# Kernel optimization log

Measured on AMD Instinct MI355X. Metric: run time of the kernel, lower is better.

The kernel has to match this reference:

```python
import jax, jax.numpy as jnp
import numpy as np

B, C, H, W = 4, 256, 64, 64
IC = C // 2  # inter_channels default = in_channels // 2


def setup_inputs() -> dict:
    key = jax.random.key(0)
    ks = jax.random.split(key, 7)
    x = jax.random.normal(ks[0], (B, C, H, W), dtype=jnp.float32)
    s = 0.02
    Wq = jax.random.normal(ks[1], (IC, C), dtype=jnp.float32) * s
    bq = jnp.zeros((IC,), dtype=jnp.float32)
    Wk = jax.random.normal(ks[2], (IC, C), dtype=jnp.float32) * s
    bk = jnp.zeros((IC,), dtype=jnp.float32)
    Wv = jax.random.normal(ks[3], (C, C), dtype=jnp.float32) * s
    bv = jnp.zeros((C,), dtype=jnp.float32)
    gamma = jnp.full((1,), 0.1, dtype=jnp.float32)  # nn.Parameter; init 0 in torch, 0.1 here for nontrivial grads
    return {"x": x, "Wq": Wq, "bq": bq, "Wk": Wk, "bk": bk, "Wv": Wv, "bv": bv, "gamma": gamma}


def reference(x, Wq, bq, Wk, bk, Wv, bv, gamma):
    b, c, h, w = x.shape
    n = h * w
    # 1x1 conv projections == per-pixel linear layers
    q = jnp.einsum('bchw,oc->bohw', x, Wq) + bq[None, :, None, None]  # [B,IC,H,W]
    k = jnp.einsum('bchw,oc->bohw', x, Wk) + bk[None, :, None, None]
    v = jnp.einsum('bchw,oc->bohw', x, Wv) + bv[None, :, None, None]  # [B,C,H,W]
    q = q.reshape(b, IC, n).transpose(0, 2, 1)  # [B,N,IC]
    k = k.reshape(b, IC, n)                     # [B,IC,N]
    v = v.reshape(b, c, n)                      # [B,C,N]
    scale = jnp.asarray(IC, x.dtype) ** -0.5
    energy = jnp.einsum('bni,bim->bnm', q, k) * scale  # [B,N,N]
    attn = jax.nn.softmax(energy, axis=-1)             # dropout is identity in eval
    # torch: out = bmm(value, attention.transpose(-1,-2)) -> out[b,c,i] = sum_j v[b,c,j]*attn[b,i,j]
    out = jnp.einsum('bcj,bij->bci', v, attn).reshape(b, c, h, w)
    return gamma[0] * out + 2.0 * x
```

## Files before the change

### kernel.cpp

```cpp
#include <hip/hip_runtime.h>
#include <stdint.h>


#define Bn 4
#define Cn 256
#define ICn 128
#define Nn 4096

typedef __attribute__((ext_vector_type(8))) short bf16x8;
typedef __attribute__((ext_vector_type(4))) float f32x4;
typedef __attribute__((ext_vector_type(16))) float f32x16;
typedef __attribute__((ext_vector_type(8))) int i32x8;

#define SCALE1 0x7f7f7f7f

__device__ __forceinline__ unsigned short f2bf(float f) {
  union { float f; uint32_t u; } v; v.f = f;
  uint32_t r = (v.u + 0x7fffu + ((v.u >> 16) & 1u)) >> 16;
  return (unsigned short)r;
}

__device__ __forceinline__ uint32_t pk4_fp8(float a, float b, float c, float d) {
  int r = 0;
  r = __builtin_amdgcn_cvt_pk_fp8_f32(a, b, r, false);
  r = __builtin_amdgcn_cvt_pk_fp8_f32(c, d, r, true);
  return (uint32_t)r;
}

__global__ __launch_bounds__(256) void cvt_weights(const float* __restrict__ Wq,
                                                   const float* __restrict__ Wk,
                                                   const float* __restrict__ Wv,
                                                   unsigned short* __restrict__ wbf) {
  int t = blockIdx.x * 256 + threadIdx.x;
  int tile = t >> 9;
  int kk = (t >> 6) & 7;
  int lane = t & 63;
  const float* W; int row;
  if (tile < 8)       { W = Wq; row = tile * 16 + (lane & 15); }
  else if (tile < 16) { W = Wk; row = (tile - 8) * 16 + (lane & 15); }
  else                { W = Wv; row = (tile - 16) * 16 + (lane & 15); }
  const float* src = W + (size_t)row * Cn + kk * 32 + (lane >> 4) * 8;
  float4 f0 = *(const float4*)src;
  float4 f1 = *(const float4*)(src + 4);
  ushort4 o0, o1;
  o0.x = f2bf(f0.x); o0.y = f2bf(f0.y); o0.z = f2bf(f0.z); o0.w = f2bf(f0.w);
  o1.x = f2bf(f1.x); o1.y = f2bf(f1.y); o1.z = f2bf(f1.z); o1.w = f2bf(f1.w);
  *(ushort4*)(wbf + (size_t)t * 8)     = o0;
  *(ushort4*)(wbf + (size_t)t * 8 + 4) = o1;
}

__global__ __launch_bounds__(256, 2) void proj_kernel(const float* __restrict__ x,
                                                      const unsigned short* __restrict__ wbf,
                                                      const float* __restrict__ bq,
                                                      const float* __restrict__ bk,
                                                      const float* __restrict__ bv,
                                                      uint8_t* __restrict__ qF,
                                                      uint8_t* __restrict__ kF,
                                                      uint8_t* __restrict__ vF) {
  const int b = blockIdx.y;
  const int ntile = blockIdx.x;
  const int px0 = ntile * 32;
  const int tid = threadIdx.x;
  const int lane = tid & 63;
  const int w = tid >> 6;
  const int c0 = lane & 15, g = lane >> 4;
  const float hscale = 0.3570958292f;

  __shared__ __align__(16) unsigned short xT[32][264];
  __shared__ __align__(16) uint8_t tb[4][4096];

  #pragma unroll
  for (int t = 0; t < 8; ++t) {
    int c = (tid >> 3) + t * 32;
    int i8 = tid & 7;
    float4 f4 = *(const float4*)(x + ((size_t)(b * Cn + c)) * Nn + px0 + i8 * 4);
    xT[i8 * 4 + 0][c] = f2bf(f4.x);
    xT[i8 * 4 + 1][c] = f2bf(f4.y);
    xT[i8 * 4 + 2][c] = f2bf(f4.z);
    xT[i8 * 4 + 3][c] = f2bf(f4.w);
  }
  __syncthreads();

  bf16x8 a[2][8];
  #pragma unroll
  for (int h = 0; h < 2; ++h)
    #pragma unroll
    for (int kk = 0; kk < 8; ++kk)
      a[h][kk] = *(const bf16x8*)&xT[h * 16 + c0][kk * 32 + g * 8];

  f32x4 zero = {0.f, 0.f, 0.f, 0.f};
  uint8_t* tw = &tb[w][0];

  if (w < 2) {
    const int isq = (w == 0);
    const float* bias = isq ? bq : bk;
    uint8_t* dst = isq ? qF : kF;
    #pragma unroll
    for (int otl = 0; otl < 8; ++otl) {
      const int wt = (isq ? 0 : 8) + otl;
      bf16x8 wf[8];
      #pragma unroll
      for (int kk = 0; kk < 8; ++kk)
        wf[kk] = *(const bf16x8*)(wbf + (((size_t)wt * 8 + kk) << 9) + lane * 8);
      float4 bz = *(const float4*)(bias + otl * 16 + g * 4);
      #pragma unroll
      for (int h = 0; h < 2; ++h) {
        f32x4 acc = zero;
        #pragma unroll
        for (int kk = 0; kk < 8; ++kk)
          acc = __builtin_amdgcn_mfma_f32_16x16x32_bf16(wf[kk], a[h][kk], acc, 0, 0, 0);
        uint32_t d = pk4_fp8((acc[0] + bz.x) * hscale, (acc[1] + bz.y) * hscale,
                             (acc[2] + bz.z) * hscale, (acc[3] + bz.w) * hscale);
        int D = otl * 4 + g;
        int off = ((D >> 4) << 11) + (((((D >> 3) & 1) << 5) + h * 16 + c0) << 5) + ((D & 7) << 2);
        *(uint32_t*)(tw + off) = d;
      }
    }
    size_t base = ((size_t)(b * 128 + ntile)) << 12;
    #pragma unroll
    for (int r = 0; r < 4; ++r) {
      uint4 v = *(const uint4*)(tw + r * 1024 + lane * 16);
      *(uint4*)(dst + base + r * 1024 + lane * 16) = v;
    }
  } else {
    #pragma unroll
    for (int oi = 0; oi < 8; ++oi) {
      const int vtg = (w - 2) * 8 + oi;
      bf16x8 wf[8];
      #pragma unroll
      for (int kk = 0; kk < 8; ++kk)
        wf[kk] = *(const bf16x8*)(wbf + (((size_t)(16 + vtg) * 8 + kk) << 9) + lane * 8);
      const float bias = bv[vtg * 16 + c0];
      #pragma unroll
      for (int h = 0; h < 2; ++h) {
        f32x4 acc = zero;
        #pragma unroll
        for (int kk = 0; kk < 8; ++kk)
          acc = __builtin_amdgcn_mfma_f32_16x16x32_bf16(a[h][kk], wf[kk], acc, 0, 0, 0);
        uint32_t d = pk4_fp8(acc[0] + bias, acc[1] + bias, acc[2] + bias, acc[3] + bias);
        int off = (((vtg >> 1) & 3) << 10) + ((((vtg & 1) << 4) + c0) << 5) + ((h * 4 + g) << 2);
        *(uint32_t*)(tw + off) = d;
      }
    }
    const int ctb = (w - 2) * 4;
    size_t base0 = (((size_t)(b * 64 + (ntile >> 1)) * 8 + ctb) << 11)
                 + (size_t)(((ntile & 1) << 5) << 5);
    #pragma unroll
    for (int r = 0; r < 2; ++r) {
      int ctl = r * 2 + (lane >> 5);
      int li = lane & 31;
      const uint8_t* s = tw + r * 2048 + lane * 32;
      uint4 v0 = *(const uint4*)(s);
      uint4 v1 = *(const uint4*)(s + 16);
      uint8_t* gp = vF + base0 + ((size_t)ctl << 11) + li * 32;
      *(uint4*)(gp) = v0;
      *(uint4*)(gp + 16) = v1;
    }
  }
}

__global__ __launch_bounds__(256, 2) void attn_kernel(const uint8_t* __restrict__ qF,
                                                      const uint8_t* __restrict__ kF,
                                                      const uint8_t* __restrict__ vF,
                                                      const float* __restrict__ x,
                                                      const float* __restrict__ gamma,
                                                      float* __restrict__ out) {
  const int blk = blockIdx.x;
  const int b = (blk & 7) >> 1;
  const int rg = (blk >> 3) | ((blk & 1) << 6);
  const int n0 = rg * 32;
  const int ph = (blk >> 3) & 15;
  const int tid = threadIdx.x;
  const int L = tid & 63;
  const int ks = tid >> 6;
  const int l31 = L & 31, l5 = L >> 5;
  const bool lo = (l5 == 0);

  __shared__ __align__(16) struct SM {
    float obuf[256][33];
    float lsum[4][32];
  } sm;

  i32x8 qv[2];
  {
    const uint8_t* qp = qF + ((size_t)(b * 128 + rg) * 2) * 2048 + L * 32;
    #pragma unroll
    for (int mf = 0; mf < 2; ++mf) {
      union { uint4 u[2]; i32x8 v; } u;
      u.u[0] = *(const uint4*)(qp + mf * 2048);
      u.u[1] = *(const uint4*)(qp + mf * 2048 + 16);
      qv[mf] = u.v;
    }
  }

  f32x16 oacc[8];
  #pragma unroll
  for (int ct = 0; ct < 8; ++ct)
    #pragma unroll
    for (int i = 0; i < 16; ++i) oacc[ct][i] = 0.f;
  float lacc = 0.f;

  const uint8_t* kBase = kF + ((size_t)(b * 128) * 2) * 2048 + L * 32;
  const uint8_t* vBase = vF + ((size_t)(b * 64) * 8) * 2048 + L * 32;

  for (int it = 0; it < 16; ++it) {
    const int kb = ks * 16 + ((it + ph) & 15);

    i32x8 kv[4];
    {
      const uint8_t* kp = kBase + (size_t)kb * 8192;
      #pragma unroll
      for (int f = 0; f < 4; ++f) {
        union { uint4 u[2]; i32x8 v; } u;
        u.u[0] = *(const uint4*)(kp + f * 2048);
        u.u[1] = *(const uint4*)(kp + f * 2048 + 16);
        kv[f] = u.v;
      }
    }

    const uint8_t* vp = vBase + (size_t)kb * 16384;
    uint4 vA[8], vB[8];
    #pragma unroll
    for (int ct = 0; ct < 8; ++ct) vA[ct] = *(const uint4*)(vp + ct * 2048);

    f32x16 s;
    #pragma unroll
    for (int i = 0; i < 16; ++i) s[i] = 0.f;
    s = __builtin_amdgcn_mfma_scale_f32_32x32x64_f8f6f4(kv[0], qv[0], s, 0, 0, 0, SCALE1, 0, SCALE1);
    s = __builtin_amdgcn_mfma_scale_f32_32x32x64_f8f6f4(kv[1], qv[1], s, 0, 0, 0, SCALE1, 0, SCALE1);
    #pragma unroll
    for (int i = 0; i < 16; ++i) {
      float r;
      asm("v_exp_f32 %0, %1" : "=v"(r) : "v"(s[i]));
      s[i] = r;
    }
    #pragma unroll
    for (int i = 0; i < 16; ++i) lacc += s[i];
    uint32_t d0 = pk4_fp8(s[0], s[1], s[2], s[3]);
    uint32_t d1 = pk4_fp8(s[4], s[5], s[6], s[7]);
    uint32_t d2 = pk4_fp8(s[8], s[9], s[10], s[11]);
    uint32_t d3 = pk4_fp8(s[12], s[13], s[14], s[15]);

    #pragma unroll
    for (int i = 0; i < 16; ++i) s[i] = 0.f;
    s = __builtin_amdgcn_mfma_scale_f32_32x32x64_f8f6f4(kv[2], qv[0], s, 0, 0, 0, SCALE1, 0, SCALE1);
    s = __builtin_amdgcn_mfma_scale_f32_32x32x64_f8f6f4(kv[3], qv[1], s, 0, 0, 0, SCALE1, 0, SCALE1);

    #pragma unroll
    for (int ct = 0; ct < 8; ++ct) vB[ct] = *(const uint4*)(vp + ct * 2048 + 16);

    #pragma unroll
    for (int i = 0; i < 16; ++i) {
      float r;
      asm("v_exp_f32 %0, %1" : "=v"(r) : "v"(s[i]));
      s[i] = r;
    }
    #pragma unroll
    for (int i = 0; i < 16; ++i) lacc += s[i];
    uint32_t e0 = pk4_fp8(s[0], s[1], s[2], s[3]);
    uint32_t e1 = pk4_fp8(s[4], s[5], s[6], s[7]);
    uint32_t e2 = pk4_fp8(s[8], s[9], s[10], s[11]);
    uint32_t e3 = pk4_fp8(s[12], s[13], s[14], s[15]);

    union { uint32_t w[8]; i32x8 v; } pf;
    {
      uint32_t a0 = e0, b0 = d0;
      asm("v_permlane32_swap_b32 %0, %1" : "+v"(a0), "+v"(b0));
      pf.w[0] = b0; pf.w[1] = a0;
      uint32_t a1 = e1, b1 = d1;
      asm("v_permlane32_swap_b32 %0, %1" : "+v"(a1), "+v"(b1));
      pf.w[2] = b1; pf.w[3] = a1;
      uint32_t a2 = e2, b2 = d2;
      asm("v_permlane32_swap_b32 %0, %1" : "+v"(a2), "+v"(b2));
      pf.w[4] = b2; pf.w[5] = a2;
      uint32_t a3 = e3, b3 = d3;
      asm("v_permlane32_swap_b32 %0, %1" : "+v"(a3), "+v"(b3));
      pf.w[6] = b3; pf.w[7] = a3;
    }

    #pragma unroll
    for (int ct = 0; ct < 8; ++ct) {
      union { uint4 u[2]; i32x8 v; } va;
      va.u[0] = vA[ct]; va.u[1] = vB[ct];
      oacc[ct] = __builtin_amdgcn_mfma_scale_f32_32x32x64_f8f6f4(va.v, pf.v, oacc[ct], 0, 0, 0, SCALE1, 0, SCALE1);
    }
  }

  float lfin = lacc + __shfl_xor(lacc, 32, 64);

  #pragma unroll
  for (int pq = 0; pq < 4; ++pq) {
    __syncthreads();
    if (pq == 0 && lo) sm.lsum[ks][l31] = lfin;
    if (ks == pq) {
      #pragma unroll
      for (int ct = 0; ct < 8; ++ct) {
        #pragma unroll
        for (int i = 0; i < 16; ++i) {
          int ch = ct * 32 + (i & 3) + 8 * (i >> 2) + 4 * l5;
          if (pq == 0) sm.obuf[ch][l31] = oacc[ct][i];
          else         sm.obuf[ch][l31] += oacc[ct][i];
        }
      }
    }
  }
  __syncthreads();

  const int row = tid & 31;
  const float coef = gamma[0] / (sm.lsum[0][row] + sm.lsum[1][row] +
                                 sm.lsum[2][row] + sm.lsum[3][row]);
  #pragma unroll 4
  for (int t = 0; t < 32; ++t) {
    int ch = (tid >> 5) + t * 8;
    size_t off = ((size_t)(b * Cn + ch)) * Nn + n0 + row;
    out[off] = sm.obuf[ch][row] * coef + 2.0f * x[off];
  }
}

extern "C" void kernel_launch(void* const* d_in, const int* in_sizes, int n_in,
                              void* d_out, int out_size, void* d_ws, size_t ws_size,
                              hipStream_t stream) {
  const float* x     = (const float*)d_in[0];
  const float* Wq    = (const float*)d_in[1];
  const float* bq    = (const float*)d_in[2];
  const float* Wk    = (const float*)d_in[3];
  const float* bk    = (const float*)d_in[4];
  const float* Wv    = (const float*)d_in[5];
  const float* bv    = (const float*)d_in[6];
  const float* gamma = (const float*)d_in[7];
  float* out = (float*)d_out;

  uint8_t* qF = (uint8_t*)d_ws;
  uint8_t* kF = qF + (2u << 20);
  uint8_t* vF = kF + (2u << 20);
  unsigned short* wbf = (unsigned short*)(vF + (4u << 20));

  hipLaunchKernelGGL(cvt_weights, dim3(64), dim3(256), 0, stream, Wq, Wk, Wv, wbf);
  hipLaunchKernelGGL(proj_kernel, dim3(128, 4), dim3(256), 0, stream,
                     x, wbf, bq, bk, bv, qF, kF, vF);
  hipLaunchKernelGGL(attn_kernel, dim3(512), dim3(256), 0, stream,
                     qF, kF, vF, x, gamma, out);
}
```

Measured before the change: 128.8 us.

## Double-buffer K in registers and stream V into LDS asynchronously

Restructures the attention main loop into a software pipeline. The next iteration's K fragments are prefetched into a second register set while the current one computes. The first half of each V tile is copied global-to-LDS with global_load_lds into a per-wave double buffer, issued after the PV MFMAs. The aim is to hide global load latency behind the QK and PV MFMAs and the exp work. In exchange the kernel uses more LDS (a 64KB union shared with the epilogue buffer), which could limit occupancy, and it relies on the compiler waiting correctly on the asynchronous LDS writes.

```diff
diff --git a/kernel.cpp b/kernel.cpp
--- a/kernel.cpp
+++ b/kernel.cpp
@@ -25,6 +25,11 @@
   r = __builtin_amdgcn_cvt_pk_fp8_f32(a, b, r, false);
   r = __builtin_amdgcn_cvt_pk_fp8_f32(c, d, r, true);
   return (uint32_t)r;
+}
+
+__device__ __forceinline__ void glds16(const uint8_t* g, uint8_t* l) {
+  __builtin_amdgcn_global_load_lds((const __attribute__((address_space(1))) void*)g,
+                                   (__attribute__((address_space(3))) void*)l, 16, 0, 0);
 }
 
 __global__ __launch_bounds__(256) void cvt_weights(const float* __restrict__ Wq,
@@ -159,6 +164,102 @@
   }
 }
 
+template <int P, bool PRE>
+__device__ __forceinline__ void attn_body(int it, int ks, int ph, int L,
+                                          const uint8_t* kBase, const uint8_t* vGsrc,
+                                          uint8_t* vst_w, const i32x8 (&qv)[2],
+                                          i32x8 (&kv0)[4], i32x8 (&kv1)[4],
+                                          f32x16 (&oacc)[8], float& lacc) {
+  i32x8 (&kvP)[4] = P ? kv1 : kv0;
+  i32x8 (&kvN)[4] = P ? kv0 : kv1;
+  const int kb = ks * 16 + ((it + ph) & 15);
+  const int kbn = ks * 16 + ((it + 1 + ph) & 15);
+  const uint8_t* vp = vGsrc + (size_t)kb * 16384;
+
+  f32x16 s;
+  #pragma unroll
+  for (int i = 0; i < 16; ++i) s[i] = 0.f;
+  s = __builtin_amdgcn_mfma_scale_f32_32x32x64_f8f6f4(kvP[0], qv[0], s, 0, 0, 0, SCALE1, 0, SCALE1);
+  s = __builtin_amdgcn_mfma_scale_f32_32x32x64_f8f6f4(kvP[1], qv[1], s, 0, 0, 0, SCALE1, 0, SCALE1);
+  #pragma unroll
+  for (int i = 0; i < 16; ++i) {
+    float r;
+    asm("v_exp_f32 %0, %1" : "=v"(r) : "v"(s[i]));
+    s[i] = r;
+  }
+  #pragma unroll
+  for (int i = 0; i < 16; ++i) lacc += s[i];
+  uint32_t d0 = pk4_fp8(s[0], s[1], s[2], s[3]);
+  uint32_t d1 = pk4_fp8(s[4], s[5], s[6], s[7]);
+  uint32_t d2 = pk4_fp8(s[8], s[9], s[10], s[11]);
+  uint32_t d3 = pk4_fp8(s[12], s[13], s[14], s[15]);
+
+  #pragma unroll
+  for (int i = 0; i < 16; ++i) s[i] = 0.f;
+  s = __builtin_amdgcn_mfma_scale_f32_32x32x64_f8f6f4(kvP[2], qv[0], s, 0, 0, 0, SCALE1, 0, SCALE1);
+  s = __builtin_amdgcn_mfma_scale_f32_32x32x64_f8f6f4(kvP[3], qv[1], s, 0, 0, 0, SCALE1, 0, SCALE1);
+
+  uint4 vB[8];
+  #pragma unroll
+  for (int ct = 0; ct < 8; ++ct) vB[ct] = *(const uint4*)(vp + ct * 2048 + 16);
+
+  if constexpr (PRE) {
+    const uint8_t* kp = kBase + (size_t)kbn * 8192;
+    #pragma unroll
+    for (int f = 0; f < 4; ++f) {
+      union { uint4 u[2]; i32x8 v; } u;
+      u.u[0] = *(const uint4*)(kp + f * 2048);
+      u.u[1] = *(const uint4*)(kp + f * 2048 + 16);
+      kvN[f] = u.v;
+    }
+  }
+
+  #pragma unroll
+  for (int i = 0; i < 16; ++i) {
+    float r;
+    asm("v_exp_f32 %0, %1" : "=v"(r) : "v"(s[i]));
+    s[i] = r;
+  }
+  #pragma unroll
+  for (int i = 0; i < 16; ++i) lacc += s[i];
+  uint32_t e0 = pk4_fp8(s[0], s[1], s[2], s[3]);
+  uint32_t e1 = pk4_fp8(s[4], s[5], s[6], s[7]);
+  uint32_t e2 = pk4_fp8(s[8], s[9], s[10], s[11]);
+  uint32_t e3 = pk4_fp8(s[12], s[13], s[14], s[15]);
+
+  union { uint32_t w[8]; i32x8 v; } pf;
+  {
+    uint32_t a0 = e0, b0 = d0;
+    asm("v_permlane32_swap_b32 %0, %1" : "+v"(a0), "+v"(b0));
+    pf.w[0] = b0; pf.w[1] = a0;
+    uint32_t a1 = e1, b1 = d1;
+    asm("v_permlane32_swap_b32 %0, %1" : "+v"(a1), "+v"(b1));
+    pf.w[2] = b1; pf.w[3] = a1;
+    uint32_t a2 = e2, b2 = d2;
+    asm("v_permlane32_swap_b32 %0, %1" : "+v"(a2), "+v"(b2));
+    pf.w[4] = b2; pf.w[5] = a2;
+    uint32_t a3 = e3, b3 = d3;
+    asm("v_permlane32_swap_b32 %0, %1" : "+v"(a3), "+v"(b3));
+    pf.w[6] = b3; pf.w[7] = a3;
+  }
+
+  #pragma unroll
+  for (int ct = 0; ct < 8; ++ct) {
+    union { uint4 u[2]; i32x8 v; } va;
+    va.u[0] = *(const uint4*)(vst_w + P * 8192 + ct * 1024 + (size_t)L * 16);
+    va.u[1] = vB[ct];
+    oacc[ct] = __builtin_amdgcn_mfma_scale_f32_32x32x64_f8f6f4(va.v, pf.v, oacc[ct], 0, 0, 0, SCALE1, 0, SCALE1);
+  }
+
+  if constexpr (PRE) {
+    const uint8_t* vpn = vGsrc + (size_t)kbn * 16384;
+    uint8_t* ldst = vst_w + (P ^ 1) * 8192;
+    #pragma unroll
+    for (int ct = 0; ct < 8; ++ct)
+      glds16(vpn + ct * 2048, ldst + ct * 1024);
+  }
+}
+
 __global__ __launch_bounds__(256, 2) void attn_kernel(const uint8_t* __restrict__ qF,
                                                       const uint8_t* __restrict__ kF,
                                                       const uint8_t* __restrict__ vF,
@@ -176,9 +277,9 @@
   const int l31 = L & 31, l5 = L >> 5;
   const bool lo = (l5 == 0);
 
-  __shared__ __align__(16) struct SM {
-    float obuf[256][33];
-    float lsum[4][32];
+  __shared__ __align__(16) union SM {
+    uint8_t vst[4][2][8192];
+    struct { float obuf[256][33]; float lsum[4][32]; } e;
   } sm;
 
   i32x8 qv[2];
@@ -201,105 +302,48 @@
   float lacc = 0.f;
 
   const uint8_t* kBase = kF + ((size_t)(b * 128) * 2) * 2048 + L * 32;
-  const uint8_t* vBase = vF + ((size_t)(b * 64) * 8) * 2048 + L * 32;
-
-  for (int it = 0; it < 16; ++it) {
-    const int kb = ks * 16 + ((it + ph) & 15);
-
-    i32x8 kv[4];
-    {
-      const uint8_t* kp = kBase + (size_t)kb * 8192;
-      #pragma unroll
-      for (int f = 0; f < 4; ++f) {
-        union { uint4 u[2]; i32x8 v; } u;
-        u.u[0] = *(const uint4*)(kp + f * 2048);
-        u.u[1] = *(const uint4*)(kp + f * 2048 + 16);
-        kv[f] = u.v;
-      }
-    }
-
-    const uint8_t* vp = vBase + (size_t)kb * 16384;
-    uint4 vA[8], vB[8];
-    #pragma unroll
-    for (int ct = 0; ct < 8; ++ct) vA[ct] = *(const uint4*)(vp + ct * 2048);
-
-    f32x16 s;
-    #pragma unroll
-    for (int i = 0; i < 16; ++i) s[i] = 0.f;
-    s = __builtin_amdgcn_mfma_scale_f32_32x32x64_f8f6f4(kv[0], qv[0], s, 0, 0, 0, SCALE1, 0, SCALE1);
-    s = __builtin_amdgcn_mfma_scale_f32_32x32x64_f8f6f4(kv[1], qv[1], s, 0, 0, 0, SCALE1, 0, SCALE1);
-    #pragma unroll
-    for (int i = 0; i < 16; ++i) {
-      float r;
-      asm("v_exp_f32 %0, %1" : "=v"(r) : "v"(s[i]));
-      s[i] = r;
-    }
-    #pragma unroll
-    for (int i = 0; i < 16; ++i) lacc += s[i];
-    uint32_t d0 = pk4_fp8(s[0], s[1], s[2], s[3]);
-    uint32_t d1 = pk4_fp8(s[4], s[5], s[6], s[7]);
-    uint32_t d2 = pk4_fp8(s[8], s[9], s[10], s[11]);
-    uint32_t d3 = pk4_fp8(s[12], s[13], s[14], s[15]);
-
-    #pragma unroll
-    for (int i = 0; i < 16; ++i) s[i] = 0.f;
-    s = __builtin_amdgcn_mfma_scale_f32_32x32x64_f8f6f4(kv[2], qv[0], s, 0, 0, 0, SCALE1, 0, SCALE1);
-    s = __builtin_amdgcn_mfma_scale_f32_32x32x64_f8f6f4(kv[3], qv[1], s, 0, 0, 0, SCALE1, 0, SCALE1);
-
-    #pragma unroll
-    for (int ct = 0; ct < 8; ++ct) vB[ct] = *(const uint4*)(vp + ct * 2048 + 16);
-
-    #pragma unroll
-    for (int i = 0; i < 16; ++i) {
-      float r;
-      asm("v_exp_f32 %0, %1" : "=v"(r) : "v"(s[i]));
-      s[i] = r;
-    }
-    #pragma unroll
-    for (int i = 0; i < 16; ++i) lacc += s[i];
-    uint32_t e0 = pk4_fp8(s[0], s[1], s[2], s[3]);
-    uint32_t e1 = pk4_fp8(s[4], s[5], s[6], s[7]);
-    uint32_t e2 = pk4_fp8(s[8], s[9], s[10], s[11]);
-    uint32_t e3 = pk4_fp8(s[12], s[13], s[14], s[15]);
-
-    union { uint32_t w[8]; i32x8 v; } pf;
-    {
-      uint32_t a0 = e0, b0 = d0;
-      asm("v_permlane32_swap_b32 %0, %1" : "+v"(a0), "+v"(b0));
-      pf.w[0] = b0; pf.w[1] = a0;
-      uint32_t a1 = e1, b1 = d1;
-      asm("v_permlane32_swap_b32 %0, %1" : "+v"(a1), "+v"(b1));
-      pf.w[2] = b1; pf.w[3] = a1;
-      uint32_t a2 = e2, b2 = d2;
-      asm("v_permlane32_swap_b32 %0, %1" : "+v"(a2), "+v"(b2));
-      pf.w[4] = b2; pf.w[5] = a2;
-      uint32_t a3 = e3, b3 = d3;
-      asm("v_permlane32_swap_b32 %0, %1" : "+v"(a3), "+v"(b3));
-      pf.w[6] = b3; pf.w[7] = a3;
-    }
-
-    #pragma unroll
-    for (int ct = 0; ct < 8; ++ct) {
-      union { uint4 u[2]; i32x8 v; } va;
-      va.u[0] = vA[ct]; va.u[1] = vB[ct];
-      oacc[ct] = __builtin_amdgcn_mfma_scale_f32_32x32x64_f8f6f4(va.v, pf.v, oacc[ct], 0, 0, 0, SCALE1, 0, SCALE1);
-    }
-  }
+  const uint8_t* vGsrc = vF + ((size_t)(b * 64) * 8) * 2048 + L * 32;
+  uint8_t* vst_w = &sm.vst[tid >> 6][0][0];
+
+  i32x8 kv0[4], kv1[4];
+
+  {
+    const int kb0 = ks * 16 + ph;
+    const uint8_t* vp0 = vGsrc + (size_t)kb0 * 16384;
+    #pragma unroll
+    for (int ct = 0; ct < 8; ++ct)
+      glds16(vp0 + ct * 2048, vst_w + ct * 1024);
+    const uint8_t* kp = kBase + (size_t)kb0 * 8192;
+    #pragma unroll
+    for (int f = 0; f < 4; ++f) {
+      union { uint4 u[2]; i32x8 v; } u;
+      u.u[0] = *(const uint4*)(kp + f * 2048);
+      u.u[1] = *(const uint4*)(kp + f * 2048 + 16);
+      kv0[f] = u.v;
+    }
+  }
+
+  for (int i2 = 0; i2 < 7; ++i2) {
+    attn_body<0, true>(2 * i2,     ks, ph, L, kBase, vGsrc, vst_w, qv, kv0, kv1, oacc, lacc);
+    attn_body<1, true>(2 * i2 + 1, ks, ph, L, kBase, vGsrc, vst_w, qv, kv0, kv1, oacc, lacc);
+  }
+  attn_body<0, true>(14, ks, ph, L, kBase, vGsrc, vst_w, qv, kv0, kv1, oacc, lacc);
+  attn_body<1, false>(15, ks, ph, L, kBase, vGsrc, vst_w, qv, kv0, kv1, oacc, lacc);
 
   float lfin = lacc + __shfl_xor(lacc, 32, 64);
 
   #pragma unroll
   for (int pq = 0; pq < 4; ++pq) {
     __syncthreads();
-    if (pq == 0 && lo) sm.lsum[ks][l31] = lfin;
+    if (pq == 0 && lo) sm.e.lsum[ks][l31] = lfin;
     if (ks == pq) {
       #pragma unroll
       for (int ct = 0; ct < 8; ++ct) {
         #pragma unroll
         for (int i = 0; i < 16; ++i) {
           int ch = ct * 32 + (i & 3) + 8 * (i >> 2) + 4 * l5;
-          if (pq == 0) sm.obuf[ch][l31] = oacc[ct][i];
-          else         sm.obuf[ch][l31] += oacc[ct][i];
+          if (pq == 0) sm.e.obuf[ch][l31] = oacc[ct][i];
+          else         sm.e.obuf[ch][l31] += oacc[ct][i];
         }
       }
     }
@@ -307,13 +351,13 @@
   __syncthreads();
 
   const int row = tid & 31;
-  const float coef = gamma[0] / (sm.lsum[0][row] + sm.lsum[1][row] +
-                                 sm.lsum[2][row] + sm.lsum[3][row]);
+  const float coef = gamma[0] / (sm.e.lsum[0][row] + sm.e.lsum[1][row] +
+                                 sm.e.lsum[2][row] + sm.e.lsum[3][row]);
   #pragma unroll 4
   for (int t = 0; t < 32; ++t) {
     int ch = (tid >> 5) + t * 8;
     size_t off = ((size_t)(b * Cn + ch)) * Nn + n0 + row;
-    out[off] = sm.obuf[ch][row] * coef + 2.0f * x[off];
+    out[off] = sm.e.obuf[ch][row] * coef + 2.0f * x[off];
   }
 }
 
```

Result: slower. 209.7 us (+62.7%).

## Double-buffer first half of V tiles in LDS via async global_load_lds prefetch

Applied to the files above, without the earlier changes.

The first 16-byte half of each V fragment is now prefetched one iteration ahead, straight from global memory into a per-wave double-buffered LDS region using global_load_lds. It is read back from LDS just before the PV MFMAs, and the second half is now issued at the top of the iteration. The aim is to hide V load latency behind the QK/exp work and to free the VGPRs that held the vA registers. The cost is 64KB of LDS per block, shared through a union with the epilogue buffers, which may limit occupancy. Correctness depends on the compiler inserting the right vmcnt waits before the LDS reads.

```diff
diff --git a/kernel.cpp b/kernel.cpp
--- a/kernel.cpp
+++ b/kernel.cpp
@@ -25,6 +25,11 @@
   r = __builtin_amdgcn_cvt_pk_fp8_f32(a, b, r, false);
   r = __builtin_amdgcn_cvt_pk_fp8_f32(c, d, r, true);
   return (uint32_t)r;
+}
+
+__device__ __forceinline__ void glds16(const uint8_t* g, uint8_t* l) {
+  __builtin_amdgcn_global_load_lds((const __attribute__((address_space(1))) void*)g,
+                                   (__attribute__((address_space(3))) void*)l, 16, 0, 0);
 }
 
 __global__ __launch_bounds__(256) void cvt_weights(const float* __restrict__ Wq,
@@ -176,9 +181,9 @@
   const int l31 = L & 31, l5 = L >> 5;
   const bool lo = (l5 == 0);
 
-  __shared__ __align__(16) struct SM {
-    float obuf[256][33];
-    float lsum[4][32];
+  __shared__ __align__(16) union SM {
+    uint8_t vst[4][2][8192];
+    struct { float obuf[256][33]; float lsum[4][32]; } e;
   } sm;
 
   i32x8 qv[2];
@@ -202,9 +207,20 @@
 
   const uint8_t* kBase = kF + ((size_t)(b * 128) * 2) * 2048 + L * 32;
   const uint8_t* vBase = vF + ((size_t)(b * 64) * 8) * 2048 + L * 32;
+  uint8_t* vst_w = &sm.vst[tid >> 6][0][0];
+
+  {
+    const int kb0 = ks * 16 + ph;
+    const uint8_t* vp0 = vBase + (size_t)kb0 * 16384;
+    #pragma unroll
+    for (int ct = 0; ct < 8; ++ct)
+      glds16(vp0 + ct * 2048, vst_w + ct * 1024);
+  }
 
   for (int it = 0; it < 16; ++it) {
+    const int cur = it & 1;
     const int kb = ks * 16 + ((it + ph) & 15);
+    const uint8_t* vp = vBase + (size_t)kb * 16384;
 
     i32x8 kv[4];
     {
@@ -218,10 +234,9 @@
       }
     }
 
-    const uint8_t* vp = vBase + (size_t)kb * 16384;
-    uint4 vA[8], vB[8];
-    #pragma unroll
-    for (int ct = 0; ct < 8; ++ct) vA[ct] = *(const uint4*)(vp + ct * 2048);
+    uint4 vB[8];
+    #pragma unroll
+    for (int ct = 0; ct < 8; ++ct) vB[ct] = *(const uint4*)(vp + ct * 2048 + 16);
 
     f32x16 s;
     #pragma unroll
@@ -245,9 +260,6 @@
     for (int i = 0; i < 16; ++i) s[i] = 0.f;
     s = __builtin_amdgcn_mfma_scale_f32_32x32x64_f8f6f4(kv[2], qv[0], s, 0, 0, 0, SCALE1, 0, SCALE1);
     s = __builtin_amdgcn_mfma_scale_f32_32x32x64_f8f6f4(kv[3], qv[1], s, 0, 0, 0, SCALE1, 0, SCALE1);
-
-    #pragma unroll
-    for (int ct = 0; ct < 8; ++ct) vB[ct] = *(const uint4*)(vp + ct * 2048 + 16);
 
     #pragma unroll
     for (int i = 0; i < 16; ++i) {
@@ -281,8 +293,18 @@
     #pragma unroll
     for (int ct = 0; ct < 8; ++ct) {
       union { uint4 u[2]; i32x8 v; } va;
-      va.u[0] = vA[ct]; va.u[1] = vB[ct];
+      va.u[0] = *(const uint4*)(vst_w + cur * 8192 + ct * 1024 + (size_t)L * 16);
+      va.u[1] = vB[ct];
       oacc[ct] = __builtin_amdgcn_mfma_scale_f32_32x32x64_f8f6f4(va.v, pf.v, oacc[ct], 0, 0, 0, SCALE1, 0, SCALE1);
+    }
+
+    if (it < 15) {
+      const int kbn = ks * 16 + ((it + 1 + ph) & 15);
+      const uint8_t* vpn = vBase + (size_t)kbn * 16384;
+      uint8_t* ldst = vst_w + (cur ^ 1) * 8192;
+      #pragma unroll
+      for (int ct = 0; ct < 8; ++ct)
+        glds16(vpn + ct * 2048, ldst + ct * 1024);
     }
   }
 
@@ -291,15 +313,15 @@
   #pragma unroll
   for (int pq = 0; pq < 4; ++pq) {
     __syncthreads();
-    if (pq == 0 && lo) sm.lsum[ks][l31] = lfin;
+    if (pq == 0 && lo) sm.e.lsum[ks][l31] = lfin;
     if (ks == pq) {
       #pragma unroll
       for (int ct = 0; ct < 8; ++ct) {
         #pragma unroll
         for (int i = 0; i < 16; ++i) {
           int ch = ct * 32 + (i & 3) + 8 * (i >> 2) + 4 * l5;
-          if (pq == 0) sm.obuf[ch][l31] = oacc[ct][i];
-          else         sm.obuf[ch][l31] += oacc[ct][i];
+          if (pq == 0) sm.e.obuf[ch][l31] = oacc[ct][i];
+          else         sm.e.obuf[ch][l31] += oacc[ct][i];
         }
       }
     }
@@ -307,13 +329,13 @@
   __syncthreads();
 
   const int row = tid & 31;
-  const float coef = gamma[0] / (sm.lsum[0][row] + sm.lsum[1][row] +
-                                 sm.lsum[2][row] + sm.lsum[3][row]);
+  const float coef = gamma[0] / (sm.e.lsum[0][row] + sm.e.lsum[1][row] +
+                                 sm.e.lsum[2][row] + sm.e.lsum[3][row]);
   #pragma unroll 4
   for (int t = 0; t < 32; ++t) {
     int ch = (tid >> 5) + t * 8;
     size_t off = ((size_t)(b * Cn + ch)) * Nn + n0 + row;
-    out[off] = sm.obuf[ch][row] * coef + 2.0f * x[off];
+    out[off] = sm.e.obuf[ch][row] * coef + 2.0f * x[off];
   }
 }
 
```

Result: slower. 143.1 us (+11.1%).
